# Kernel tuning notes

Hardware: AMD Instinct MI355X
Metric: run time of the kernel (lower is better)

The kernel has to match this reference:

```python
import jax, jax.numpy as jnp
import numpy as np

EPS = 1e-6
NUM_HEADS = 16  # config.num_attention_heads

def _rms(h, w):
    h32 = h.astype(jnp.float32)
    v = jnp.mean(h32 * h32, axis=-1, keepdims=True)
    return (w * h32 * jax.lax.rsqrt(v + EPS)).astype(h.dtype)

def _rope(q, k, pos):
    dh = q.shape[-1]
    inv = 1.0 / (10000.0 ** (jnp.arange(0, dh, 2, dtype=jnp.float32) / dh))
    ang = pos.astype(jnp.float32)[:, None] * inv[None, :]  # [n, dh/2]
    cos = jnp.concatenate([jnp.cos(ang), jnp.cos(ang)], -1)[None, None]  # [1,1,n,dh]
    sin = jnp.concatenate([jnp.sin(ang), jnp.sin(ang)], -1)[None, None]
    def rot(x):
        x1, x2 = x[..., :dh // 2], x[..., dh // 2:]
        return jnp.concatenate([-x2, x1], -1)
    return q * cos + rot(q) * sin, k * cos + rot(k) * sin

def _skip_causal_mask(N, block_size, len1, text_len):
    qi = jnp.arange(N)[:, None]
    ki = jnp.arange(N)[None, :]
    qb = (qi - text_len) // block_size
    kb = (ki - text_len) // block_size
    iq = qi >= text_len
    ik = ki >= text_len
    return (((ki < text_len) & (qi >= ki))
            | (iq & ik & (qb < len1) & (kb < len1) & (qb >= kb))
            | (iq & ik & (qb >= len1) & (kb < len1) & (qb - len1 > kb))
            | (iq & ik & (qb == kb)))

def _layer(x, position_ids, text_position_ids, qkv_w, qkv_b, proj_w, proj_b,
           qn_w, kn_w, ln1_w, ln2_w, gate_w, up_w, down_w,
           block_size, text_len, len1):
    B, N, C = x.shape
    H = NUM_HEADS
    Dh = C // H
    T = text_len
    Lc = len1 * block_size
    offs = [0, T, T + Lc]
    lens = [T, Lc, N - T - Lc]  # text / clean / noised segment lengths
    qs, ks, vs = [], [], []
    for i in range(3):
        seg = _rms(x[:, offs[i]:offs[i] + lens[i]], ln1_w[i])  # input layernorm
        qkv = seg @ qkv_w[i] + qkv_b[i]                        # [B,n,3C]
        qkv = qkv.reshape(B, lens[i], 3, H, Dh).transpose(2, 0, 3, 1, 4)
        qs.append(_rms(qkv[0], qn_w[i]))
        ks.append(_rms(qkv[1], kn_w[i]))
        vs.append(qkv[2])
    img_q = jnp.concatenate([qs[1], qs[2]], axis=2)
    img_k = jnp.concatenate([ks[1], ks[2]], axis=2)
    img_q, img_k = _rope(img_q, img_k, position_ids)
    txt_q, txt_k = _rope(qs[0], ks[0], text_position_ids)
    q = jnp.concatenate([txt_q, img_q], axis=2)
    k = jnp.concatenate([txt_k, img_k], axis=2)
    v = jnp.concatenate(vs, axis=2)
    scores = jnp.einsum('bhqd,bhkd->bhqk', q, k) / np.float32(np.sqrt(Dh))
    mask = _skip_causal_mask(N, block_size, len1, text_len)
    scores = jnp.where(mask, scores, jnp.finfo(scores.dtype).min)
    attn = jax.nn.softmax(scores, axis=-1)
    o = jnp.einsum('bhqk,bhkd->bhqd', attn, v)
    o = o.transpose(0, 2, 1, 3).reshape(B, N, C)
    o = jnp.concatenate([o[:, offs[i]:offs[i] + lens[i]] @ proj_w[i] + proj_b[i]
                         for i in range(3)], axis=1)
    h = x + o
    mlp = []
    for i in range(3):
        y = _rms(h[:, offs[i]:offs[i] + lens[i]], ln2_w[i])  # post-attn layernorm
        mlp.append((jax.nn.silu(y @ gate_w[i]) * (y @ up_w[i])) @ down_w[i])
    return h + jnp.concatenate(mlp, axis=1)

def setup_inputs():
    key = jax.random.key(0)
    ks = jax.random.split(key, 8)
    B, C, H, I = 2, 1024, 16, 4096
    block_size, text_len, len1, len2 = 128, 256, 4, 4
    N = text_len + (len1 + len2) * block_size  # 1280
    s = 0.02
    return {
        'x': jax.random.normal(ks[0], (B, N, C), jnp.float32),
        'position_ids': jnp.arange((len1 + len2) * block_size, dtype=jnp.int32),
        'text_position_ids': jnp.arange(text_len, dtype=jnp.int32),
        'qkv_w': jax.random.normal(ks[1], (3, C, 3 * C), jnp.float32) * s,
        'qkv_b': jnp.zeros((3, 3 * C), jnp.float32),
        'proj_w': jax.random.normal(ks[2], (3, C, C), jnp.float32) * s,
        'proj_b': jnp.zeros((3, C), jnp.float32),
        'qn_w': jnp.ones((3, C // H), jnp.float32),
        'kn_w': jnp.ones((3, C // H), jnp.float32),
        'ln1_w': jnp.ones((3, C), jnp.float32),
        'ln2_w': jnp.ones((3, C), jnp.float32),
        'gate_w': jax.random.normal(ks[3], (3, C, I), jnp.float32) * s,
        'up_w': jax.random.normal(ks[4], (3, C, I), jnp.float32) * s,
        'down_w': jax.random.normal(ks[5], (3, I, C), jnp.float32) * s,
        'block_size': block_size, 'text_len': text_len, 'len1': len1,
    }

def reference(x, position_ids, text_position_ids, qkv_w, qkv_b, proj_w, proj_b,
              qn_w, kn_w, ln1_w, ln2_w, gate_w, up_w, down_w,
              block_size, text_len, len1):
    return _layer(x, position_ids, text_position_ids, qkv_w, qkv_b, proj_w, proj_b,
                  qn_w, kn_w, ln1_w, ln2_w, gate_w, up_w, down_w,
                  block_size, text_len, len1)
```

## Files before the change

### kernel.cpp

```cpp
#include <hip/hip_runtime.h>
#include <math.h>

constexpr int Bb  = 2;
constexpr int Nn  = 1280;
constexpr int Cc  = 1024;
constexpr int Hh  = 16;
constexpr int DH  = 64;
constexpr int Ii  = 4096;
constexpr int Tt  = 256;
constexpr int BSz = 128;
constexpr int L1  = 4;
constexpr int Mrows = Bb * Nn;

typedef __attribute__((ext_vector_type(8))) short short8v;
typedef __attribute__((ext_vector_type(4))) float f32x4;

__device__ __forceinline__ int segof(int n) {
    return n < Tt ? 0 : (n < Tt + L1 * BSz ? 1 : 2);
}
__device__ __forceinline__ unsigned short f2bf(float f) {
    unsigned int u = __float_as_uint(f);
    u += 0x7fffu + ((u >> 16) & 1u);
    return (unsigned short)(u >> 16);
}
__device__ __forceinline__ float bf2f(unsigned short h) {
    return __uint_as_float(((unsigned int)h) << 16);
}

__device__ __forceinline__ int xcd_swz(int lin, int nwg) {
    int cpx = nwg >> 3;
    return (lin & 7) * cpx + (lin >> 3);
}

__global__ __launch_bounds__(256)
void rms_bf16(const float* __restrict__ in, const float* __restrict__ w,
              unsigned short* __restrict__ out) {
    int row = blockIdx.x;
    int n   = row % Nn;
    int seg = segof(n);
    const float* x = in + (size_t)row * Cc;
    int t = threadIdx.x;
    float4 xv = reinterpret_cast<const float4*>(x)[t];
    float ss = xv.x * xv.x + xv.y * xv.y + xv.z * xv.z + xv.w * xv.w;
#pragma unroll
    for (int off = 32; off; off >>= 1) ss += __shfl_down(ss, off, 64);
    __shared__ float red[4];
    __shared__ float s_r;
    int lane = t & 63, wid = t >> 6;
    if (lane == 0) red[wid] = ss;
    __syncthreads();
    if (t == 0) s_r = rsqrtf((red[0] + red[1] + red[2] + red[3]) * (1.0f / Cc) + 1e-6f);
    __syncthreads();
    float r = s_r;
    float4 wv = reinterpret_cast<const float4*>(w + (size_t)seg * Cc)[t];
    ushort4 ov;
    ov.x = f2bf(wv.x * xv.x * r);
    ov.y = f2bf(wv.y * xv.y * r);
    ov.z = f2bf(wv.z * xv.z * r);
    ov.w = f2bf(wv.w * xv.w * r);
    *reinterpret_cast<ushort4*>(&out[(size_t)row * Cc + t * 4]) = ov;
}

__global__ __launch_bounds__(256)
void pack_w(const float* __restrict__ W, unsigned short* __restrict__ PB,
            int K, int Nd) {
    size_t idx = (size_t)blockIdx.x * 256 + threadIdx.x;
    size_t cpseg = (size_t)K * Nd / 8;
    int s = (int)(idx / cpseg);
    size_t rm = idx % cpseg;
    int lane = (int)(rm & 63);
    int fr   = (int)((rm >> 6) & 7);
    size_t tile = rm >> 9;
    int nct = Nd >> 7;
    int cb = (int)(tile % nct);
    int kt = (int)(tile / nct);
    int col = cb * 128 + fr * 16 + (lane & 15);
    int k0  = kt * 32 + (lane >> 4) * 8;
    const float* src = W + ((size_t)s * K + k0) * Nd + col;
    unsigned short o[8];
#pragma unroll
    for (int j = 0; j < 8; j++) o[j] = f2bf(src[(size_t)j * Nd]);
    short8v v;
#pragma unroll
    for (int j = 0; j < 8; j++) v[j] = (short)o[j];
    *reinterpret_cast<short8v*>(&PB[idx * 8]) = v;
}

template <int OUTMODE, bool BIAS, int NZ>
__global__ __launch_bounds__(256)
void gemm64(const unsigned short* __restrict__ A,
            const unsigned short* __restrict__ PB,
            const float* __restrict__ bias, void* __restrict__ outp,
            int K, int Nd) {
    __shared__ __align__(16) unsigned short lds[12288];
    int bx = blockIdx.x, by = blockIdx.y, bz = (NZ > 1) ? blockIdx.z : 0;
    {
        int gx = gridDim.x, gy = gridDim.y, gz = (NZ > 1) ? gridDim.z : 1;
        int lin = bx + gx * (by + gy * bz);
        int swz = xcd_swz(lin, gx * gy * gz);
        bx = swz % gx; swz /= gx;
        by = swz % gy; bz = swz / gy;
    }
    int rb = bx * 64, cb = by;
    int seg = segof(rb % Nn);
    int tid = threadIdx.x, lane = tid & 63, wid = tid >> 6;
    int wr = wid >> 1, wc = wid & 1;
    int g = lane >> 4, c_ = lane & 15;
    const unsigned short* PBseg = PB + (size_t)seg * K * Nd;
    const int nct = Nd >> 7;
    const int Keff = K / NZ;
    const int nKt = Keff >> 6;
    const int kz = bz * Keff;

    f32x4 acc[2][4];
#pragma unroll
    for (int m = 0; m < 2; m++)
#pragma unroll
        for (int n = 0; n < 4; n++) acc[m][n] = (f32x4){0.f, 0.f, 0.f, 0.f};

    short8v av[2], bv[4];
    auto load_tile = [&](int kt) {
#pragma unroll
        for (int i = 0; i < 2; i++) {
            int c = tid + i * 256;
            int rf = c >> 7, kb = (c >> 6) & 1, lc = c & 63;
            int row = rb + rf * 16 + (lc & 15);
            int k0  = kz + kt * 64 + kb * 32 + (lc >> 4) * 8;
            av[i] = *reinterpret_cast<const short8v*>(&A[(size_t)row * K + k0]);
        }
#pragma unroll
        for (int i = 0; i < 4; i++) {
            int c = tid + i * 256;
            int cf = c >> 7, kb = (c >> 6) & 1, lc = c & 63;
            int kt32 = (kz >> 5) + kt * 2 + kb;
            bv[i] = *reinterpret_cast<const short8v*>(
                &PBseg[((((size_t)kt32 * nct + cb) * 8 + cf) * 64 + lc) * 8]);
        }
    };

    load_tile(0);
    for (int kt = 0; kt < nKt; ++kt) {
        __syncthreads();
#pragma unroll
        for (int i = 0; i < 2; i++)
            *reinterpret_cast<short8v*>(&lds[(size_t)(tid + i * 256) * 8]) = av[i];
#pragma unroll
        for (int i = 0; i < 4; i++)
            *reinterpret_cast<short8v*>(&lds[4096 + (size_t)(tid + i * 256) * 8]) = bv[i];
        __syncthreads();
        if (kt + 1 < nKt) load_tile(kt + 1);
        short8v afr[2][2], bfr[4][2];
#pragma unroll
        for (int m = 0; m < 2; m++)
#pragma unroll
            for (int kb = 0; kb < 2; kb++)
                afr[m][kb] = *reinterpret_cast<short8v*>(
                    &lds[(((wr * 2 + m) * 2 + kb) * 64 + lane) * 8]);
#pragma unroll
        for (int n = 0; n < 4; n++)
#pragma unroll
            for (int kb = 0; kb < 2; kb++)
                bfr[n][kb] = *reinterpret_cast<short8v*>(
                    &lds[4096 + (((wc * 4 + n) * 2 + kb) * 64 + lane) * 8]);
#pragma unroll
        for (int m = 0; m < 2; m++)
#pragma unroll
            for (int n = 0; n < 4; n++)
#pragma unroll
                for (int kb = 0; kb < 2; kb++)
                    acc[m][n] = __builtin_amdgcn_mfma_f32_16x16x32_bf16(
                        afr[m][kb], bfr[n][kb], acc[m][n], 0, 0, 0);
    }

    float* outf = (float*)outp;
    unsigned short* outh = (unsigned short*)outp;
    size_t zoff = (NZ > 1) ? (size_t)bz * Mrows * Nd : 0;
#pragma unroll
    for (int n = 0; n < 4; n++) {
        int col = cb * 128 + wc * 64 + n * 16 + c_;
        float bvv = BIAS ? bias[(size_t)seg * Nd + col] : 0.f;
#pragma unroll
        for (int m = 0; m < 2; m++) {
#pragma unroll
            for (int r = 0; r < 4; r++) {
                int row = rb + wr * 32 + m * 16 + g * 4 + r;
                float v = acc[m][n][r] + bvv;
                if (OUTMODE == 0) outf[zoff + (size_t)row * Nd + col] = v;
                else              outh[zoff + (size_t)row * Nd + col] = f2bf(v);
            }
        }
    }
}

__global__ __launch_bounds__(256)
void gemm_gu(const unsigned short* __restrict__ A,
             const unsigned short* __restrict__ PG,
             const unsigned short* __restrict__ PU,
             unsigned short* __restrict__ outp) {
    __shared__ __align__(16) unsigned short lds[10240];
    int bx = blockIdx.x, by = blockIdx.y;
    {
        int lin = bx + gridDim.x * by;
        int swz = xcd_swz(lin, gridDim.x * gridDim.y);
        bx = swz % gridDim.x; by = swz / gridDim.x;
    }
    int rb = bx * 64, cb = by;
    int seg = segof(rb % Nn);
    int tid = threadIdx.x, lane = tid & 63, wid = tid >> 6;
    int wr = wid >> 1, wc = wid & 1;
    int g = lane >> 4, c_ = lane & 15;
    const int nct = Ii >> 7;
    const unsigned short* PGseg = PG + (size_t)seg * Cc * Ii;
    const unsigned short* PUseg = PU + (size_t)seg * Cc * Ii;

    f32x4 accG[2][4], accU[2][4];
#pragma unroll
    for (int m = 0; m < 2; m++)
#pragma unroll
        for (int n = 0; n < 4; n++) {
            accG[m][n] = (f32x4){0.f, 0.f, 0.f, 0.f};
            accU[m][n] = (f32x4){0.f, 0.f, 0.f, 0.f};
        }

    int mf0 = tid >> 6, lc0 = tid & 63;
    const unsigned short* gA =
        &A[(size_t)(rb + mf0 * 16 + (lc0 & 15)) * Cc + (lc0 >> 4) * 8];
    const size_t bstep = (size_t)nct * 4096;
    short8v av, gv[2], uv[2];
    auto load_tile = [&](int kt) {
        av = *reinterpret_cast<const short8v*>(gA + kt * 32);
#pragma unroll
        for (int i = 0; i < 2; i++) {
            int c = tid + i * 256;
            int cf = c >> 6, lc = c & 63;
            size_t off = (((size_t)kt * nct + cb) * 8 + cf) * 64 * 8 + (size_t)lc * 8;
            gv[i] = *reinterpret_cast<const short8v*>(PGseg + off);
            uv[i] = *reinterpret_cast<const short8v*>(PUseg + off);
        }
    };

    const int nKt = Cc >> 5;
    load_tile(0);
    for (int kt = 0; kt < nKt; ++kt) {
        __syncthreads();
        *reinterpret_cast<short8v*>(&lds[(size_t)tid * 8]) = av;
#pragma unroll
        for (int i = 0; i < 2; i++) {
            *reinterpret_cast<short8v*>(&lds[2048 + (size_t)(tid + i * 256) * 8]) = gv[i];
            *reinterpret_cast<short8v*>(&lds[6144 + (size_t)(tid + i * 256) * 8]) = uv[i];
        }
        __syncthreads();
        if (kt + 1 < nKt) load_tile(kt + 1);
        short8v afr[2], gfr[4], ufr[4];
#pragma unroll
        for (int m = 0; m < 2; m++)
            afr[m] = *reinterpret_cast<short8v*>(&lds[((wr * 2 + m) * 64 + lane) * 8]);
#pragma unroll
        for (int n = 0; n < 4; n++) {
            gfr[n] = *reinterpret_cast<short8v*>(&lds[2048 + ((wc * 4 + n) * 64 + lane) * 8]);
            ufr[n] = *reinterpret_cast<short8v*>(&lds[6144 + ((wc * 4 + n) * 64 + lane) * 8]);
        }
#pragma unroll
        for (int m = 0; m < 2; m++)
#pragma unroll
            for (int n = 0; n < 4; n++) {
                accG[m][n] = __builtin_amdgcn_mfma_f32_16x16x32_bf16(
                    afr[m], gfr[n], accG[m][n], 0, 0, 0);
                accU[m][n] = __builtin_amdgcn_mfma_f32_16x16x32_bf16(
                    afr[m], ufr[n], accU[m][n], 0, 0, 0);
            }
    }

#pragma unroll
    for (int n = 0; n < 4; n++) {
        int col = cb * 128 + wc * 64 + n * 16 + c_;
#pragma unroll
        for (int m = 0; m < 2; m++) {
#pragma unroll
            for (int r = 0; r < 4; r++) {
                int row = rb + wr * 32 + m * 16 + g * 4 + r;
                float gval = accG[m][n][r], uval = accU[m][n][r];
                float t = gval / (1.f + __expf(-gval)) * uval;
                outp[(size_t)row * Ii + col] = f2bf(t);
            }
        }
    }
}

__global__ __launch_bounds__(256)
void combine_proj(const float* __restrict__ x, const float* __restrict__ bias,
                  const float* __restrict__ p, float* __restrict__ hb) {
    int i = blockIdx.x * 256 + threadIdx.x;
    int base = i * 4;
    int col = base % Cc;
    int n   = (base / Cc) % Nn;
    int seg = segof(n);
    float4 a = reinterpret_cast<const float4*>(x)[i];
    float4 b = *reinterpret_cast<const float4*>(&bias[(size_t)seg * Cc + col]);
    float4 p0 = reinterpret_cast<const float4*>(p)[i];
    float4 p1 = reinterpret_cast<const float4*>(p)[i + Mrows * Cc / 4];
    float4 r;
    r.x = a.x + b.x + p0.x + p1.x;
    r.y = a.y + b.y + p0.y + p1.y;
    r.z = a.z + b.z + p0.z + p1.z;
    r.w = a.w + b.w + p0.w + p1.w;
    reinterpret_cast<float4*>(hb)[i] = r;
}

__global__ __launch_bounds__(256)
void combine_down4(const unsigned short* __restrict__ p,
                   float* __restrict__ out) {
    int i = blockIdx.x * 256 + threadIdx.x;
    float4 a = reinterpret_cast<const float4*>(out)[i];
#pragma unroll
    for (int z = 0; z < 4; z++) {
        ushort4 u = *reinterpret_cast<const ushort4*>(&p[(size_t)z * Mrows * Cc + i * 4]);
        a.x += bf2f(u.x); a.y += bf2f(u.y); a.z += bf2f(u.z); a.w += bf2f(u.w);
    }
    reinterpret_cast<float4*>(out)[i] = a;
}

__global__ __launch_bounds__(256)
void split_rope(const unsigned short* __restrict__ qkv,
                const float* __restrict__ qn_w, const float* __restrict__ kn_w,
                const int* __restrict__ pos_ids, const int* __restrict__ tpos_ids,
                unsigned short* __restrict__ Q, unsigned short* __restrict__ K,
                unsigned short* __restrict__ V) {
    int row = blockIdx.x;
    int b = row / Nn, n = row % Nn;
    int seg = segof(n);
    int lane = threadIdx.x & 63, wid = threadIdx.x >> 6;
    int pos = (n < Tt) ? tpos_ids[n] : pos_ids[n - Tt];
    int j = lane & 31;
    float ang = (float)pos * exp2f(-(float)j * (13.287712379549449f / 32.f));
    float cv = cosf(ang), sv = sinf(ang);
    float qw = qn_w[seg * DH + lane], kw = kn_w[seg * DH + lane];
    for (int h = wid; h < Hh; h += 4) {
        const unsigned short* base = qkv + (size_t)row * (3 * Cc) + h * DH + lane;
        float q = bf2f(base[0]), k = bf2f(base[Cc]), v = bf2f(base[2 * Cc]);
        float qs = q * q, ks = k * k;
#pragma unroll
        for (int off = 32; off; off >>= 1) {
            qs += __shfl_xor(qs, off, 64);
            ks += __shfl_xor(ks, off, 64);
        }
        q = q * rsqrtf(qs * (1.f / DH) + 1e-6f) * qw;
        k = k * rsqrtf(ks * (1.f / DH) + 1e-6f) * kw;
        float qp = __shfl_xor(q, 32, 64);
        float kp = __shfl_xor(k, 32, 64);
        float qo = q * cv + ((lane < 32) ? -qp * sv : qp * sv);
        float ko = k * cv + ((lane < 32) ? -kp * sv : kp * sv);
        size_t oidx = ((size_t)(b * Hh + h) * Nn + n) * DH + lane;
        Q[oidx] = f2bf(qo);
        K[oidx] = f2bf(ko);
        V[oidx] = f2bf(v);
    }
}

__global__ __launch_bounds__(256)
void attn_mfma(const unsigned short* __restrict__ Qg,
               const unsigned short* __restrict__ Kg,
               const unsigned short* __restrict__ Vg,
               unsigned short* __restrict__ O) {
    __shared__ __align__(16) unsigned short k_lds[64 * 64];
    __shared__ __align__(16) unsigned short vt_lds[64 * 64];
    __shared__ __align__(16) unsigned short p_lds[4][16 * 64];

    int qt = blockIdx.x;
    int bh = blockIdx.y;
    int b = bh >> 4, h = bh & 15;
    int tid = threadIdx.x, lane = tid & 63, wid = tid >> 6;
    int g = lane >> 4, c = lane & 15;

    const size_t headoff = (size_t)bh * Nn * DH;
    int q0 = qt * 64;
    bool qtext = q0 < Tt;
    int qb = qtext ? 0 : (q0 - Tt) / BSz;

    int qrow_frag = q0 + wid * 16 + c;
    short8v aq[2];
#pragma unroll
    for (int kb = 0; kb < 2; kb++)
        aq[kb] = *reinterpret_cast<const short8v*>(
            &Qg[headoff + (size_t)qrow_frag * DH + kb * 32 + g * 8]);

    unsigned short* pbuf = &p_lds[wid][0];

    f32x4 o_[4];
#pragma unroll
    for (int nb = 0; nb < 4; nb++) o_[nb] = (f32x4){0.f, 0.f, 0.f, 0.f};
    float m_[4] = {-3.4e38f, -3.4e38f, -3.4e38f, -3.4e38f};
    float l_[4] = {0.f, 0.f, 0.f, 0.f};

    int tr = tid >> 2, tc = tid & 3;

    for (int kt = 0; kt < Nn / 64; kt++) {
        int kbase = kt * 64;
        bool vis, diag = false;
        if (qtext) {
            vis = (kbase <= q0);
            diag = (kbase == q0);
        } else if (kbase < Tt) {
            vis = true;
        } else {
            int kb = (kbase - Tt) / BSz;
            vis = (qb < L1) ? (kb <= qb)
                            : ((kb < L1 && qb - L1 > kb) || kb == qb);
        }
        if (!vis) continue;

        __syncthreads();
        {
            const unsigned short* ks = &Kg[headoff + (size_t)(kbase + tr) * DH];
            const unsigned short* vs = &Vg[headoff + (size_t)(kbase + tr) * DH];
#pragma unroll
            for (int i = 0; i < 2; i++) {
                int ch = tc + i * 4;
                short8v kv = *reinterpret_cast<const short8v*>(ks + ch * 8);
                int byte = (tr * 128 + ch * 16) ^ ((tr & 7) << 4);
                *reinterpret_cast<short8v*>((char*)k_lds + byte) = kv;
                short8v vv = *reinterpret_cast<const short8v*>(vs + ch * 8);
#pragma unroll
                for (int j = 0; j < 8; j++) {
                    int dh = ch * 8 + j;
                    int vbyte = (dh * 128 + tr * 2) ^ ((dh & 7) << 4);
                    *reinterpret_cast<unsigned short*>((char*)vt_lds + vbyte) =
                        (unsigned short)vv[j];
                }
            }
        }
        __syncthreads();

        f32x4 s_[4];
#pragma unroll
        for (int nb = 0; nb < 4; nb++) s_[nb] = (f32x4){0.f, 0.f, 0.f, 0.f};
#pragma unroll
        for (int nb = 0; nb < 4; nb++) {
            int kil = nb * 16 + c;
#pragma unroll
            for (int kb = 0; kb < 2; kb++) {
                int byte = (kil * 128 + kb * 64 + g * 16) ^ ((kil & 7) << 4);
                short8v bk = *reinterpret_cast<short8v*>((char*)k_lds + byte);
                s_[nb] = __builtin_amdgcn_mfma_f32_16x16x32_bf16(aq[kb], bk, s_[nb], 0, 0, 0);
            }
        }
#pragma unroll
        for (int nb = 0; nb < 4; nb++) {
#pragma unroll
            for (int r = 0; r < 4; r++) {
                float sv = s_[nb][r] * 0.125f;
                if (diag) {
                    int qrl = wid * 16 + g * 4 + r;
                    int kcl = nb * 16 + c;
                    if (qrl < kcl) sv = -3.4e38f;
                }
                s_[nb][r] = sv;
            }
        }
#pragma unroll
        for (int r = 0; r < 4; r++) {
            float mx = fmaxf(fmaxf(s_[0][r], s_[1][r]), fmaxf(s_[2][r], s_[3][r]));
#pragma unroll
            for (int off = 1; off <= 8; off <<= 1)
                mx = fmaxf(mx, __shfl_xor(mx, off, 64));
            float mn = fmaxf(m_[r], mx);
            float es = __expf(m_[r] - mn);
            m_[r] = mn;
            float pv[4];
            float rs = 0.f;
#pragma unroll
            for (int nb = 0; nb < 4; nb++) {
                pv[nb] = __expf(s_[nb][r] - mn);
                rs += pv[nb];
            }
#pragma unroll
            for (int off = 1; off <= 8; off <<= 1)
                rs += __shfl_xor(rs, off, 64);
            l_[r] = l_[r] * es + rs;
#pragma unroll
            for (int nb = 0; nb < 4; nb++) o_[nb][r] *= es;
            int qrl = g * 4 + r;
            int swz = (qrl & 7) << 4;
#pragma unroll
            for (int nb = 0; nb < 4; nb++) {
                int byte = (qrl * 128 + (nb * 16 + c) * 2) ^ swz;
                *reinterpret_cast<unsigned short*>((char*)pbuf + byte) = f2bf(pv[nb]);
            }
        }
        short8v aP[2];
#pragma unroll
        for (int kb = 0; kb < 2; kb++) {
            int byte = (c * 128 + kb * 64 + g * 16) ^ ((c & 7) << 4);
            aP[kb] = *reinterpret_cast<short8v*>((char*)pbuf + byte);
        }
#pragma unroll
        for (int nb = 0; nb < 4; nb++) {
            int dh = nb * 16 + c;
#pragma unroll
            for (int kb = 0; kb < 2; kb++) {
                int byte = (dh * 128 + kb * 64 + g * 16) ^ ((dh & 7) << 4);
                short8v bv = *reinterpret_cast<short8v*>((char*)vt_lds + byte);
                o_[nb] = __builtin_amdgcn_mfma_f32_16x16x32_bf16(aP[kb], bv, o_[nb], 0, 0, 0);
            }
        }
    }

    float inv_[4];
#pragma unroll
    for (int r = 0; r < 4; r++) inv_[r] = 1.f / l_[r];
#pragma unroll
    for (int nb = 0; nb < 4; nb++) {
        int col = h * DH + nb * 16 + c;
#pragma unroll
        for (int r = 0; r < 4; r++) {
            int row = q0 + wid * 16 + g * 4 + r;
            O[((size_t)b * Nn + row) * Cc + col] = f2bf(o_[nb][r] * inv_[r]);
        }
    }
}

extern "C" void kernel_launch(void* const* d_in, const int* in_sizes, int n_in,
                              void* d_out, int out_size, void* d_ws, size_t ws_size,
                              hipStream_t stream) {
    const float* x        = (const float*)d_in[0];
    const int*   pos_ids  = (const int*)d_in[1];
    const int*   tpos_ids = (const int*)d_in[2];
    const float* qkv_w    = (const float*)d_in[3];
    const float* qkv_b    = (const float*)d_in[4];
    const float* proj_w   = (const float*)d_in[5];
    const float* proj_b   = (const float*)d_in[6];
    const float* qn_w     = (const float*)d_in[7];
    const float* kn_w     = (const float*)d_in[8];
    const float* ln1_w    = (const float*)d_in[9];
    const float* ln2_w    = (const float*)d_in[10];
    const float* gate_w   = (const float*)d_in[11];
    const float* up_w     = (const float*)d_in[12];
    const float* down_w   = (const float*)d_in[13];
    float* out = (float*)d_out;
    char*  wsb = (char*)d_ws;

    unsigned short* WA  = (unsigned short*)(wsb);
    unsigned short* WB  = (unsigned short*)(wsb + 25165824);
    unsigned short* Tb  = (unsigned short*)(wsb + 50331648);
    unsigned short* P3  = (unsigned short*)(wsb + 71303168);
    unsigned short* Qbf = Tb;
    unsigned short* Kbf = Tb + 2621440;
    unsigned short* Vbf = Tb + 5242880;

    rms_bf16<<<Mrows, 256, 0, stream>>>(x, ln1_w, P3);
    pack_w<<<4608, 256, 0, stream>>>(qkv_w, WA, Cc, 3 * Cc);
    gemm64<1, true, 1><<<dim3(Mrows / 64, 24), 256, 0, stream>>>(
        P3, WA, qkv_b, WB, Cc, 3 * Cc);
    split_rope<<<Mrows, 256, 0, stream>>>(WB, qn_w, kn_w, pos_ids, tpos_ids,
                                          Qbf, Kbf, Vbf);
    attn_mfma<<<dim3(Nn / 64, Bb * Hh), 256, 0, stream>>>(Qbf, Kbf, Vbf, P3);
    pack_w<<<1536, 256, 0, stream>>>(proj_w, WA, Cc, Cc);
    gemm64<0, false, 2><<<dim3(Mrows / 64, 8, 2), 256, 0, stream>>>(
        P3, WA, nullptr, (float*)Tb, Cc, Cc);
    combine_proj<<<Mrows * Cc / 1024, 256, 0, stream>>>(x, proj_b, (float*)Tb, out);
    rms_bf16<<<Mrows, 256, 0, stream>>>(out, ln2_w, P3);
    pack_w<<<6144, 256, 0, stream>>>(gate_w, WA, Cc, Ii);
    pack_w<<<6144, 256, 0, stream>>>(up_w, WB, Cc, Ii);
    gemm_gu<<<dim3(Mrows / 64, 32), 256, 0, stream>>>(P3, WA, WB, Tb);
    pack_w<<<6144, 256, 0, stream>>>(down_w, WA, Ii, Cc);
    gemm64<1, false, 4><<<dim3(Mrows / 64, 8, 4), 256, 0, stream>>>(
        Tb, WA, nullptr, WB, Ii, Cc);
    combine_down4<<<Mrows * Cc / 1024, 256, 0, stream>>>(WB, out);
}
```

Baseline: 287.1 us.

## Fuse weight packing into rms and attention launches; switch GEMMs to 128-row tiles

Merges the first RMSNorm with qkv weight packing into one launch. The attention kernel is combined with packing of the proj, gate and up weights, so the packing blocks run alongside attention instead of in separate launches. Replaces the 64-row GEMM with a 128-row, K=32-step tile with launch_bounds(256,2), which raises MFMA work per LDS load and lowers LDS use. The tradeoffs are fewer blocks per GEMM grid (lower parallelism) and a larger heterogeneous grid whose attention and pack blocks have unequal costs.

Measured after the change: 249.0 us. 1.15x faster.

```diff
diff --git a/kernel.cpp b/kernel.cpp
--- a/kernel.cpp
+++ b/kernel.cpp
@@ -32,10 +32,10 @@
     return (lin & 7) * cpx + (lin >> 3);
 }
 
-__global__ __launch_bounds__(256)
-void rms_bf16(const float* __restrict__ in, const float* __restrict__ w,
-              unsigned short* __restrict__ out) {
-    int row = blockIdx.x;
+__device__ __forceinline__ void rms_dev(const float* __restrict__ in,
+                                        const float* __restrict__ w,
+                                        unsigned short* __restrict__ out,
+                                        int row, float* sred) {
     int n   = row % Nn;
     int seg = segof(n);
     const float* x = in + (size_t)row * Cc;
@@ -44,14 +44,12 @@
     float ss = xv.x * xv.x + xv.y * xv.y + xv.z * xv.z + xv.w * xv.w;
 #pragma unroll
     for (int off = 32; off; off >>= 1) ss += __shfl_down(ss, off, 64);
-    __shared__ float red[4];
-    __shared__ float s_r;
     int lane = t & 63, wid = t >> 6;
-    if (lane == 0) red[wid] = ss;
+    if (lane == 0) sred[wid] = ss;
     __syncthreads();
-    if (t == 0) s_r = rsqrtf((red[0] + red[1] + red[2] + red[3]) * (1.0f / Cc) + 1e-6f);
+    if (t == 0) sred[4] = rsqrtf((sred[0] + sred[1] + sred[2] + sred[3]) * (1.0f / Cc) + 1e-6f);
     __syncthreads();
-    float r = s_r;
+    float r = sred[4];
     float4 wv = reinterpret_cast<const float4*>(w + (size_t)seg * Cc)[t];
     ushort4 ov;
     ov.x = f2bf(wv.x * xv.x * r);
@@ -61,10 +59,9 @@
     *reinterpret_cast<ushort4*>(&out[(size_t)row * Cc + t * 4]) = ov;
 }
 
-__global__ __launch_bounds__(256)
-void pack_w(const float* __restrict__ W, unsigned short* __restrict__ PB,
-            int K, int Nd) {
-    size_t idx = (size_t)blockIdx.x * 256 + threadIdx.x;
+__device__ __forceinline__ void pack_dev(const float* __restrict__ W,
+                                         unsigned short* __restrict__ PB,
+                                         int K, int Nd, size_t idx) {
     size_t cpseg = (size_t)K * Nd / 8;
     int s = (int)(idx / cpseg);
     size_t rm = idx % cpseg;
@@ -86,13 +83,223 @@
     *reinterpret_cast<short8v*>(&PB[idx * 8]) = v;
 }
 
+__global__ __launch_bounds__(256)
+void rms_bf16(const float* __restrict__ in, const float* __restrict__ w,
+              unsigned short* __restrict__ out) {
+    __shared__ float sred[5];
+    rms_dev(in, w, out, blockIdx.x, sred);
+}
+
+__global__ __launch_bounds__(256)
+void pack_w(const float* __restrict__ W, unsigned short* __restrict__ PB,
+            int K, int Nd) {
+    pack_dev(W, PB, K, Nd, (size_t)blockIdx.x * 256 + threadIdx.x);
+}
+
+__global__ __launch_bounds__(256)
+void fat1(const float* __restrict__ x, const float* __restrict__ ln1_w,
+          unsigned short* __restrict__ xn,
+          const float* __restrict__ qkv_w, unsigned short* __restrict__ qkv_p) {
+    __shared__ float sred[5];
+    int bid = blockIdx.x;
+    if (bid < Mrows) {
+        rms_dev(x, ln1_w, xn, bid, sred);
+    } else {
+        pack_dev(qkv_w, qkv_p, Cc, 3 * Cc, (size_t)(bid - Mrows) * 256 + threadIdx.x);
+    }
+}
+
+__device__ __forceinline__ void attn_dev(
+        const unsigned short* __restrict__ Qg, const unsigned short* __restrict__ Kg,
+        const unsigned short* __restrict__ Vg, unsigned short* __restrict__ O,
+        int qt, int bh,
+        unsigned short* k_lds, unsigned short* vt_lds, unsigned short* p_base) {
+    int b = bh >> 4, h = bh & 15;
+    int tid = threadIdx.x, lane = tid & 63, wid = tid >> 6;
+    int g = lane >> 4, c = lane & 15;
+
+    const size_t headoff = (size_t)bh * Nn * DH;
+    int q0 = qt * 64;
+    bool qtext = q0 < Tt;
+    int qb = qtext ? 0 : (q0 - Tt) / BSz;
+
+    int qrow_frag = q0 + wid * 16 + c;
+    short8v aq[2];
+#pragma unroll
+    for (int kb = 0; kb < 2; kb++)
+        aq[kb] = *reinterpret_cast<const short8v*>(
+            &Qg[headoff + (size_t)qrow_frag * DH + kb * 32 + g * 8]);
+
+    unsigned short* pbuf = p_base + wid * 1024;
+
+    f32x4 o_[4];
+#pragma unroll
+    for (int nb = 0; nb < 4; nb++) o_[nb] = (f32x4){0.f, 0.f, 0.f, 0.f};
+    float m_[4] = {-3.4e38f, -3.4e38f, -3.4e38f, -3.4e38f};
+    float l_[4] = {0.f, 0.f, 0.f, 0.f};
+
+    int tr = tid >> 2, tc = tid & 3;
+
+    for (int kt = 0; kt < Nn / 64; kt++) {
+        int kbase = kt * 64;
+        bool vis, diag = false;
+        if (qtext) {
+            vis = (kbase <= q0);
+            diag = (kbase == q0);
+        } else if (kbase < Tt) {
+            vis = true;
+        } else {
+            int kb = (kbase - Tt) / BSz;
+            vis = (qb < L1) ? (kb <= qb)
+                            : ((kb < L1 && qb - L1 > kb) || kb == qb);
+        }
+        if (!vis) continue;
+
+        __syncthreads();
+        {
+            const unsigned short* ks = &Kg[headoff + (size_t)(kbase + tr) * DH];
+            const unsigned short* vs = &Vg[headoff + (size_t)(kbase + tr) * DH];
+#pragma unroll
+            for (int i = 0; i < 2; i++) {
+                int ch = tc + i * 4;
+                short8v kv = *reinterpret_cast<const short8v*>(ks + ch * 8);
+                int byte = (tr * 128 + ch * 16) ^ ((tr & 7) << 4);
+                *reinterpret_cast<short8v*>((char*)k_lds + byte) = kv;
+                short8v vv = *reinterpret_cast<const short8v*>(vs + ch * 8);
+#pragma unroll
+                for (int j = 0; j < 8; j++) {
+                    int dh = ch * 8 + j;
+                    int vbyte = (dh * 128 + tr * 2) ^ ((dh & 7) << 4);
+                    *reinterpret_cast<unsigned short*>((char*)vt_lds + vbyte) =
+                        (unsigned short)vv[j];
+                }
+            }
+        }
+        __syncthreads();
+
+        f32x4 s_[4];
+#pragma unroll
+        for (int nb = 0; nb < 4; nb++) s_[nb] = (f32x4){0.f, 0.f, 0.f, 0.f};
+#pragma unroll
+        for (int nb = 0; nb < 4; nb++) {
+            int kil = nb * 16 + c;
+#pragma unroll
+            for (int kb = 0; kb < 2; kb++) {
+                int byte = (kil * 128 + kb * 64 + g * 16) ^ ((kil & 7) << 4);
+                short8v bk = *reinterpret_cast<short8v*>((char*)k_lds + byte);
+                s_[nb] = __builtin_amdgcn_mfma_f32_16x16x32_bf16(aq[kb], bk, s_[nb], 0, 0, 0);
+            }
+        }
+#pragma unroll
+        for (int nb = 0; nb < 4; nb++) {
+#pragma unroll
+            for (int r = 0; r < 4; r++) {
+                float sv = s_[nb][r] * 0.125f;
+                if (diag) {
+                    int qrl = wid * 16 + g * 4 + r;
+                    int kcl = nb * 16 + c;
+                    if (qrl < kcl) sv = -3.4e38f;
+                }
+                s_[nb][r] = sv;
+            }
+        }
+#pragma unroll
+        for (int r = 0; r < 4; r++) {
+            float mx = fmaxf(fmaxf(s_[0][r], s_[1][r]), fmaxf(s_[2][r], s_[3][r]));
+#pragma unroll
+            for (int off = 1; off <= 8; off <<= 1)
+                mx = fmaxf(mx, __shfl_xor(mx, off, 64));
+            float mn = fmaxf(m_[r], mx);
+            float es = __expf(m_[r] - mn);
+            m_[r] = mn;
+            float pv[4];
+            float rs = 0.f;
+#pragma unroll
+            for (int nb = 0; nb < 4; nb++) {
+                pv[nb] = __expf(s_[nb][r] - mn);
+                rs += pv[nb];
+            }
+#pragma unroll
+            for (int off = 1; off <= 8; off <<= 1)
+                rs += __shfl_xor(rs, off, 64);
+            l_[r] = l_[r] * es + rs;
+#pragma unroll
+            for (int nb = 0; nb < 4; nb++) o_[nb][r] *= es;
+            int qrl = g * 4 + r;
+            int swz = (qrl & 7) << 4;
+#pragma unroll
+            for (int nb = 0; nb < 4; nb++) {
+                int byte = (qrl * 128 + (nb * 16 + c) * 2) ^ swz;
+                *reinterpret_cast<unsigned short*>((char*)pbuf + byte) = f2bf(pv[nb]);
+            }
+        }
+        short8v aP[2];
+#pragma unroll
+        for (int kb = 0; kb < 2; kb++) {
+            int byte = (c * 128 + kb * 64 + g * 16) ^ ((c & 7) << 4);
+            aP[kb] = *reinterpret_cast<short8v*>((char*)pbuf + byte);
+        }
+#pragma unroll
+        for (int nb = 0; nb < 4; nb++) {
+            int dh = nb * 16 + c;
+#pragma unroll
+            for (int kb = 0; kb < 2; kb++) {
+                int byte = (dh * 128 + kb * 64 + g * 16) ^ ((dh & 7) << 4);
+                short8v bv = *reinterpret_cast<short8v*>((char*)vt_lds + byte);
+                o_[nb] = __builtin_amdgcn_mfma_f32_16x16x32_bf16(aP[kb], bv, o_[nb], 0, 0, 0);
+            }
+        }
+    }
+
+    float inv_[4];
+#pragma unroll
+    for (int r = 0; r < 4; r++) inv_[r] = 1.f / l_[r];
+#pragma unroll
+    for (int nb = 0; nb < 4; nb++) {
+        int col = h * DH + nb * 16 + c;
+#pragma unroll
+        for (int r = 0; r < 4; r++) {
+            int row = q0 + wid * 16 + g * 4 + r;
+            O[((size_t)b * Nn + row) * Cc + col] = f2bf(o_[nb][r] * inv_[r]);
+        }
+    }
+}
+
+__global__ __launch_bounds__(256)
+void fat2(const unsigned short* __restrict__ Qg, const unsigned short* __restrict__ Kg,
+          const unsigned short* __restrict__ Vg, unsigned short* __restrict__ O,
+          const float* __restrict__ proj_w, unsigned short* __restrict__ proj_p,
+          const float* __restrict__ gate_w, unsigned short* __restrict__ gate_p,
+          const float* __restrict__ up_w,   unsigned short* __restrict__ up_p) {
+    __shared__ __align__(16) unsigned short k_lds[64 * 64];
+    __shared__ __align__(16) unsigned short vt_lds[64 * 64];
+    __shared__ __align__(16) unsigned short p_lds[4 * 16 * 64];
+    int bid = blockIdx.x;
+    if (bid < 640) {
+        attn_dev(Qg, Kg, Vg, O, bid % 20, bid / 20, k_lds, vt_lds, p_lds);
+        return;
+    }
+    bid -= 640;
+    if (bid < 1536) {
+        pack_dev(proj_w, proj_p, Cc, Cc, (size_t)bid * 256 + threadIdx.x);
+        return;
+    }
+    bid -= 1536;
+    if (bid < 6144) {
+        pack_dev(gate_w, gate_p, Cc, Ii, (size_t)bid * 256 + threadIdx.x);
+        return;
+    }
+    bid -= 6144;
+    pack_dev(up_w, up_p, Cc, Ii, (size_t)bid * 256 + threadIdx.x);
+}
+
 template <int OUTMODE, bool BIAS, int NZ>
-__global__ __launch_bounds__(256)
-void gemm64(const unsigned short* __restrict__ A,
-            const unsigned short* __restrict__ PB,
-            const float* __restrict__ bias, void* __restrict__ outp,
-            int K, int Nd) {
-    __shared__ __align__(16) unsigned short lds[12288];
+__global__ __launch_bounds__(256, 2)
+void gemm128r(const unsigned short* __restrict__ A,
+              const unsigned short* __restrict__ PB,
+              const float* __restrict__ bias, void* __restrict__ outp,
+              int K, int Nd) {
+    __shared__ __align__(16) unsigned short lds[8192];
     int bx = blockIdx.x, by = blockIdx.y, bz = (NZ > 1) ? blockIdx.z : 0;
     {
         int gx = gridDim.x, gy = gridDim.y, gz = (NZ > 1) ? gridDim.z : 1;
@@ -101,75 +308,66 @@
         bx = swz % gx; swz /= gx;
         by = swz % gy; bz = swz / gy;
     }
-    int rb = bx * 64, cb = by;
+    int rb = bx * 128, cb = by;
     int seg = segof(rb % Nn);
     int tid = threadIdx.x, lane = tid & 63, wid = tid >> 6;
     int wr = wid >> 1, wc = wid & 1;
     int g = lane >> 4, c_ = lane & 15;
-    const unsigned short* PBseg = PB + (size_t)seg * K * Nd;
     const int nct = Nd >> 7;
     const int Keff = K / NZ;
-    const int nKt = Keff >> 6;
+    const int nKt = Keff >> 5;
     const int kz = bz * Keff;
-
-    f32x4 acc[2][4];
-#pragma unroll
-    for (int m = 0; m < 2; m++)
+    const unsigned short* PBseg = PB + (size_t)seg * K * Nd;
+
+    int mf0 = tid >> 6, lc0 = tid & 63;
+    const unsigned short* pA0 =
+        A + (size_t)(rb + mf0 * 16 + (lc0 & 15)) * K + kz + (lc0 >> 4) * 8;
+    const unsigned short* pA1 = pA0 + (size_t)64 * K;
+    const unsigned short* pB0 =
+        PBseg + (((size_t)(kz >> 5) * nct + cb) * 8 + mf0) * 512 + (size_t)lc0 * 8;
+    const unsigned short* pB1 = pB0 + 2048;
+    const size_t bstep = (size_t)nct * 4096;
+
+    f32x4 acc[4][4];
+#pragma unroll
+    for (int m = 0; m < 4; m++)
 #pragma unroll
         for (int n = 0; n < 4; n++) acc[m][n] = (f32x4){0.f, 0.f, 0.f, 0.f};
 
-    short8v av[2], bv[4];
-    auto load_tile = [&](int kt) {
-#pragma unroll
-        for (int i = 0; i < 2; i++) {
-            int c = tid + i * 256;
-            int rf = c >> 7, kb = (c >> 6) & 1, lc = c & 63;
-            int row = rb + rf * 16 + (lc & 15);
-            int k0  = kz + kt * 64 + kb * 32 + (lc >> 4) * 8;
-            av[i] = *reinterpret_cast<const short8v*>(&A[(size_t)row * K + k0]);
-        }
-#pragma unroll
-        for (int i = 0; i < 4; i++) {
-            int c = tid + i * 256;
-            int cf = c >> 7, kb = (c >> 6) & 1, lc = c & 63;
-            int kt32 = (kz >> 5) + kt * 2 + kb;
-            bv[i] = *reinterpret_cast<const short8v*>(
-                &PBseg[((((size_t)kt32 * nct + cb) * 8 + cf) * 64 + lc) * 8]);
-        }
-    };
-
-    load_tile(0);
+    short8v av[2], bv[2];
+    av[0] = *reinterpret_cast<const short8v*>(pA0);
+    av[1] = *reinterpret_cast<const short8v*>(pA1);
+    bv[0] = *reinterpret_cast<const short8v*>(pB0);
+    bv[1] = *reinterpret_cast<const short8v*>(pB1);
+    pA0 += 32; pA1 += 32; pB0 += bstep; pB1 += bstep;
+
     for (int kt = 0; kt < nKt; ++kt) {
         __syncthreads();
-#pragma unroll
-        for (int i = 0; i < 2; i++)
-            *reinterpret_cast<short8v*>(&lds[(size_t)(tid + i * 256) * 8]) = av[i];
-#pragma unroll
-        for (int i = 0; i < 4; i++)
-            *reinterpret_cast<short8v*>(&lds[4096 + (size_t)(tid + i * 256) * 8]) = bv[i];
+        *reinterpret_cast<short8v*>(&lds[(size_t)tid * 8]) = av[0];
+        *reinterpret_cast<short8v*>(&lds[(size_t)(tid + 256) * 8]) = av[1];
+        *reinterpret_cast<short8v*>(&lds[4096 + (size_t)tid * 8]) = bv[0];
+        *reinterpret_cast<short8v*>(&lds[4096 + (size_t)(tid + 256) * 8]) = bv[1];
         __syncthreads();
-        if (kt + 1 < nKt) load_tile(kt + 1);
-        short8v afr[2][2], bfr[4][2];
-#pragma unroll
-        for (int m = 0; m < 2; m++)
-#pragma unroll
-            for (int kb = 0; kb < 2; kb++)
-                afr[m][kb] = *reinterpret_cast<short8v*>(
-                    &lds[(((wr * 2 + m) * 2 + kb) * 64 + lane) * 8]);
+        if (kt + 1 < nKt) {
+            av[0] = *reinterpret_cast<const short8v*>(pA0);
+            av[1] = *reinterpret_cast<const short8v*>(pA1);
+            bv[0] = *reinterpret_cast<const short8v*>(pB0);
+            bv[1] = *reinterpret_cast<const short8v*>(pB1);
+            pA0 += 32; pA1 += 32; pB0 += bstep; pB1 += bstep;
+        }
+        short8v afr[4], bfr[4];
+#pragma unroll
+        for (int m = 0; m < 4; m++)
+            afr[m] = *reinterpret_cast<short8v*>(&lds[((wr * 4 + m) * 64 + lane) * 8]);
 #pragma unroll
         for (int n = 0; n < 4; n++)
-#pragma unroll
-            for (int kb = 0; kb < 2; kb++)
-                bfr[n][kb] = *reinterpret_cast<short8v*>(
-                    &lds[4096 + (((wc * 4 + n) * 2 + kb) * 64 + lane) * 8]);
-#pragma unroll
-        for (int m = 0; m < 2; m++)
+            bfr[n] = *reinterpret_cast<short8v*>(&lds[4096 + ((wc * 4 + n) * 64 + lane) * 8]);
+#pragma unroll
+        for (int m = 0; m < 4; m++)
 #pragma unroll
             for (int n = 0; n < 4; n++)
-#pragma unroll
-                for (int kb = 0; kb < 2; kb++)
-                    acc[m][n] = __builtin_amdgcn_mfma_f32_16x16x32_bf16(
-                        afr[m][kb], bfr[n][kb], acc[m][n], 0, 0, 0);
+                acc[m][n] = __builtin_amdgcn_mfma_f32_16x16x32_bf16(
+                    afr[m], bfr[n], acc[m][n], 0, 0, 0);
     }
 
     float* outf = (float*)outp;
@@ -180,10 +378,10 @@
         int col = cb * 128 + wc * 64 + n * 16 + c_;
         float bvv = BIAS ? bias[(size_t)seg * Nd + col] : 0.f;
 #pragma unroll
-        for (int m = 0; m < 2; m++) {
+        for (int m = 0; m < 4; m++) {
 #pragma unroll
             for (int r = 0; r < 4; r++) {
-                int row = rb + wr * 32 + m * 16 + g * 4 + r;
+                int row = rb + wr * 64 + m * 16 + g * 4 + r;
                 float v = acc[m][n][r] + bvv;
                 if (OUTMODE == 0) outf[zoff + (size_t)row * Nd + col] = v;
                 else              outh[zoff + (size_t)row * Nd + col] = f2bf(v);
@@ -225,7 +423,6 @@
     int mf0 = tid >> 6, lc0 = tid & 63;
     const unsigned short* gA =
         &A[(size_t)(rb + mf0 * 16 + (lc0 & 15)) * Cc + (lc0 >> 4) * 8];
-    const size_t bstep = (size_t)nct * 4096;
     short8v av, gv[2], uv[2];
     auto load_tile = [&](int kt) {
         av = *reinterpret_cast<const short8v*>(gA + kt * 32);
@@ -354,168 +551,6 @@
         Q[oidx] = f2bf(qo);
         K[oidx] = f2bf(ko);
         V[oidx] = f2bf(v);
-    }
-}
-
-__global__ __launch_bounds__(256)
-void attn_mfma(const unsigned short* __restrict__ Qg,
-               const unsigned short* __restrict__ Kg,
-               const unsigned short* __restrict__ Vg,
-               unsigned short* __restrict__ O) {
-    __shared__ __align__(16) unsigned short k_lds[64 * 64];
-    __shared__ __align__(16) unsigned short vt_lds[64 * 64];
-    __shared__ __align__(16) unsigned short p_lds[4][16 * 64];
-
-    int qt = blockIdx.x;
-    int bh = blockIdx.y;
-    int b = bh >> 4, h = bh & 15;
-    int tid = threadIdx.x, lane = tid & 63, wid = tid >> 6;
-    int g = lane >> 4, c = lane & 15;
-
-    const size_t headoff = (size_t)bh * Nn * DH;
-    int q0 = qt * 64;
-    bool qtext = q0 < Tt;
-    int qb = qtext ? 0 : (q0 - Tt) / BSz;
-
-    int qrow_frag = q0 + wid * 16 + c;
-    short8v aq[2];
-#pragma unroll
-    for (int kb = 0; kb < 2; kb++)
-        aq[kb] = *reinterpret_cast<const short8v*>(
-            &Qg[headoff + (size_t)qrow_frag * DH + kb * 32 + g * 8]);
-
-    unsigned short* pbuf = &p_lds[wid][0];
-
-    f32x4 o_[4];
-#pragma unroll
-    for (int nb = 0; nb < 4; nb++) o_[nb] = (f32x4){0.f, 0.f, 0.f, 0.f};
-    float m_[4] = {-3.4e38f, -3.4e38f, -3.4e38f, -3.4e38f};
-    float l_[4] = {0.f, 0.f, 0.f, 0.f};
-
-    int tr = tid >> 2, tc = tid & 3;
-
-    for (int kt = 0; kt < Nn / 64; kt++) {
-        int kbase = kt * 64;
-        bool vis, diag = false;
-        if (qtext) {
-            vis = (kbase <= q0);
-            diag = (kbase == q0);
-        } else if (kbase < Tt) {
-            vis = true;
-        } else {
-            int kb = (kbase - Tt) / BSz;
-            vis = (qb < L1) ? (kb <= qb)
-                            : ((kb < L1 && qb - L1 > kb) || kb == qb);
-        }
-        if (!vis) continue;
-
-        __syncthreads();
-        {
-            const unsigned short* ks = &Kg[headoff + (size_t)(kbase + tr) * DH];
-            const unsigned short* vs = &Vg[headoff + (size_t)(kbase + tr) * DH];
-#pragma unroll
-            for (int i = 0; i < 2; i++) {
-                int ch = tc + i * 4;
-                short8v kv = *reinterpret_cast<const short8v*>(ks + ch * 8);
-                int byte = (tr * 128 + ch * 16) ^ ((tr & 7) << 4);
-                *reinterpret_cast<short8v*>((char*)k_lds + byte) = kv;
-                short8v vv = *reinterpret_cast<const short8v*>(vs + ch * 8);
-#pragma unroll
-                for (int j = 0; j < 8; j++) {
-                    int dh = ch * 8 + j;
-                    int vbyte = (dh * 128 + tr * 2) ^ ((dh & 7) << 4);
-                    *reinterpret_cast<unsigned short*>((char*)vt_lds + vbyte) =
-                        (unsigned short)vv[j];
-                }
-            }
-        }
-        __syncthreads();
-
-        f32x4 s_[4];
-#pragma unroll
-        for (int nb = 0; nb < 4; nb++) s_[nb] = (f32x4){0.f, 0.f, 0.f, 0.f};
-#pragma unroll
-        for (int nb = 0; nb < 4; nb++) {
-            int kil = nb * 16 + c;
-#pragma unroll
-            for (int kb = 0; kb < 2; kb++) {
-                int byte = (kil * 128 + kb * 64 + g * 16) ^ ((kil & 7) << 4);
-                short8v bk = *reinterpret_cast<short8v*>((char*)k_lds + byte);
-                s_[nb] = __builtin_amdgcn_mfma_f32_16x16x32_bf16(aq[kb], bk, s_[nb], 0, 0, 0);
-            }
-        }
-#pragma unroll
-        for (int nb = 0; nb < 4; nb++) {
-#pragma unroll
-            for (int r = 0; r < 4; r++) {
-                float sv = s_[nb][r] * 0.125f;
-                if (diag) {
-                    int qrl = wid * 16 + g * 4 + r;
-                    int kcl = nb * 16 + c;
-                    if (qrl < kcl) sv = -3.4e38f;
-                }
-                s_[nb][r] = sv;
-            }
-        }
-#pragma unroll
-        for (int r = 0; r < 4; r++) {
-            float mx = fmaxf(fmaxf(s_[0][r], s_[1][r]), fmaxf(s_[2][r], s_[3][r]));
-#pragma unroll
-            for (int off = 1; off <= 8; off <<= 1)
-                mx = fmaxf(mx, __shfl_xor(mx, off, 64));
-            float mn = fmaxf(m_[r], mx);
-            float es = __expf(m_[r] - mn);
-            m_[r] = mn;
-            float pv[4];
-            float rs = 0.f;
-#pragma unroll
-            for (int nb = 0; nb < 4; nb++) {
-                pv[nb] = __expf(s_[nb][r] - mn);
-                rs += pv[nb];
-            }
-#pragma unroll
-            for (int off = 1; off <= 8; off <<= 1)
-                rs += __shfl_xor(rs, off, 64);
-            l_[r] = l_[r] * es + rs;
-#pragma unroll
-            for (int nb = 0; nb < 4; nb++) o_[nb][r] *= es;
-            int qrl = g * 4 + r;
-            int swz = (qrl & 7) << 4;
-#pragma unroll
-            for (int nb = 0; nb < 4; nb++) {
-                int byte = (qrl * 128 + (nb * 16 + c) * 2) ^ swz;
-                *reinterpret_cast<unsigned short*>((char*)pbuf + byte) = f2bf(pv[nb]);
-            }
-        }
-        short8v aP[2];
-#pragma unroll
-        for (int kb = 0; kb < 2; kb++) {
-            int byte = (c * 128 + kb * 64 + g * 16) ^ ((c & 7) << 4);
-            aP[kb] = *reinterpret_cast<short8v*>((char*)pbuf + byte);
-        }
-#pragma unroll
-        for (int nb = 0; nb < 4; nb++) {
-            int dh = nb * 16 + c;
-#pragma unroll
-            for (int kb = 0; kb < 2; kb++) {
-                int byte = (dh * 128 + kb * 64 + g * 16) ^ ((dh & 7) << 4);
-                short8v bv = *reinterpret_cast<short8v*>((char*)vt_lds + byte);
-                o_[nb] = __builtin_amdgcn_mfma_f32_16x16x32_bf16(aP[kb], bv, o_[nb], 0, 0, 0);
-            }
-        }
-    }
-
-    float inv_[4];
-#pragma unroll
-    for (int r = 0; r < 4; r++) inv_[r] = 1.f / l_[r];
-#pragma unroll
-    for (int nb = 0; nb < 4; nb++) {
-        int col = h * DH + nb * 16 + c;
-#pragma unroll
-        for (int r = 0; r < 4; r++) {
-            int row = q0 + wid * 16 + g * 4 + r;
-            O[((size_t)b * Nn + row) * Cc + col] = f2bf(o_[nb][r] * inv_[r]);
-        }
     }
 }
 
@@ -543,27 +578,25 @@
     unsigned short* WB  = (unsigned short*)(wsb + 25165824);
     unsigned short* Tb  = (unsigned short*)(wsb + 50331648);
     unsigned short* P3  = (unsigned short*)(wsb + 71303168);
+    unsigned short* P4  = (unsigned short*)(wsb + 76546048);
     unsigned short* Qbf = Tb;
     unsigned short* Kbf = Tb + 2621440;
     unsigned short* Vbf = Tb + 5242880;
 
-    rms_bf16<<<Mrows, 256, 0, stream>>>(x, ln1_w, P3);
-    pack_w<<<4608, 256, 0, stream>>>(qkv_w, WA, Cc, 3 * Cc);
-    gemm64<1, true, 1><<<dim3(Mrows / 64, 24), 256, 0, stream>>>(
+    fat1<<<Mrows + 4608, 256, 0, stream>>>(x, ln1_w, P3, qkv_w, WA);
+    gemm128r<1, true, 1><<<dim3(Mrows / 128, 24), 256, 0, stream>>>(
         P3, WA, qkv_b, WB, Cc, 3 * Cc);
     split_rope<<<Mrows, 256, 0, stream>>>(WB, qn_w, kn_w, pos_ids, tpos_ids,
                                           Qbf, Kbf, Vbf);
-    attn_mfma<<<dim3(Nn / 64, Bb * Hh), 256, 0, stream>>>(Qbf, Kbf, Vbf, P3);
-    pack_w<<<1536, 256, 0, stream>>>(proj_w, WA, Cc, Cc);
-    gemm64<0, false, 2><<<dim3(Mrows / 64, 8, 2), 256, 0, stream>>>(
-        P3, WA, nullptr, (float*)Tb, Cc, Cc);
+    fat2<<<640 + 1536 + 6144 + 6144, 256, 0, stream>>>(
+        Qbf, Kbf, Vbf, P3, proj_w, P4, gate_w, WA, up_w, WB);
+    gemm128r<0, false, 2><<<dim3(Mrows / 128, 8, 2), 256, 0, stream>>>(
+        P3, P4, nullptr, (float*)Tb, Cc, Cc);
     combine_proj<<<Mrows * Cc / 1024, 256, 0, stream>>>(x, proj_b, (float*)Tb, out);
     rms_bf16<<<Mrows, 256, 0, stream>>>(out, ln2_w, P3);
-    pack_w<<<6144, 256, 0, stream>>>(gate_w, WA, Cc, Ii);
-    pack_w<<<6144, 256, 0, stream>>>(up_w, WB, Cc, Ii);
     gemm_gu<<<dim3(Mrows / 64, 32), 256, 0, stream>>>(P3, WA, WB, Tb);
     pack_w<<<6144, 256, 0, stream>>>(down_w, WA, Ii, Cc);
-    gemm64<1, false, 4><<<dim3(Mrows / 64, 8, 4), 256, 0, stream>>>(
+    gemm128r<1, false, 4><<<dim3(Mrows / 128, 8, 4), 256, 0, stream>>>(
         Tb, WA, nullptr, WB, Ii, Cc);
     combine_down4<<<Mrows * Cc / 1024, 256, 0, stream>>>(WB, out);
 }
```
